# Performance work log

Hardware: AMD Instinct MI355X
Metric: run time of the kernel (lower is better)

The kernel has to match this reference:

```python
import jax, jax.numpy as jnp
import numpy as np

B, H, L, D = 8, 12, 2048, 64
E = H * D            # 768 = state_size = hidden_size
K, S, P = 3, 2, 1    # conv kernel, stride, padding (2P - K = -1 matches avg_pool residual)


def setup_inputs() -> dict:
    key = jax.random.key(0)
    ks = jax.random.split(key, 8)
    init = lambda k, shape: jax.random.normal(k, shape, jnp.float32) * 0.02
    return {
        "state": jax.random.normal(ks[0], (B, H, L, D), jnp.float32),
        # input_proj Linear(E,E)
        "Wi": init(ks[1], (E, E)), "bi": jnp.zeros((E,), jnp.float32),
        # ConvMultiheadAttention: strided Conv1d query proj, stored as [K, E_in, E_out]
        "Wq": init(ks[2], (K, E, E)), "bq": jnp.zeros((E,), jnp.float32),
        "Wk": init(ks[3], (E, E)), "bk": jnp.zeros((E,), jnp.float32),
        "Wv": init(ks[4], (E, E)), "bv": jnp.zeros((E,), jnp.float32),
        "Wao": init(ks[5], (E, E)), "bao": jnp.zeros((E,), jnp.float32),  # attn out_proj
        # output_proj Linear(E,E)
        "Wo": init(ks[6], (E, E)), "bo": jnp.zeros((E,), jnp.float32),
    }


def reference(state, Wi, bi, Wq, bq, Wk, bk, Wv, bv, Wao, bao, Wo, bo):
    b, h, l, d = state.shape
    e = h * d
    # [B,H,L,D] -> [B,L,H*D]
    x = state.transpose(0, 2, 1, 3).reshape(b, l, e)
    residual = x
    # input projection + ReLU
    x = jax.nn.relu(x @ Wi.T + bi)
    # strided convolutional query projection: [B,L,E] -> [B,Lq,E]
    q = jax.lax.conv_general_dilated(
        x, Wq, window_strides=(S,), padding=[(P, P)],
        dimension_numbers=("NWC", "WIO", "NWC")) + bq
    k = x @ Wk.T + bk
    v = x @ Wv.T + bv
    lq = q.shape[1]
    qh = q.reshape(b, lq, h, d)
    kh = k.reshape(b, l, h, d)
    vh = v.reshape(b, l, h, d)
    scale = 1.0 / jnp.sqrt(jnp.asarray(d, x.dtype))
    scores = jnp.einsum("bqhd,bkhd->bhqk", qh, kh) * scale  # [B,H,Lq,L]
    attn = jax.nn.softmax(scores, axis=-1)
    o = jnp.einsum("bhqk,bkhd->bqhd", attn, vh).reshape(b, lq, e)
    o = o @ Wao.T + bao          # attention out_proj
    o = jax.nn.relu(o)
    o = o @ Wo.T + bo            # output projection
    # avg_pool1d with kernel=1, stride=S, pad=0 == strided subsampling
    o = o + residual[:, ::S, :]
    # [B,Lq,E] -> [B,H,Lq,D]
    out = o.reshape(b, lq, h, d).transpose(0, 2, 1, 3)
    return out
```

## Files before the change

kernel.cpp:

```cpp
#include <hip/hip_runtime.h>
#include <hip/hip_bf16.h>
#include <stdint.h>

#define DEVI __device__ __forceinline__

typedef short s8v __attribute__((ext_vector_type(8)));
typedef float f4v __attribute__((ext_vector_type(4)));

DEVI short f2bf(float f) {
  unsigned u = __builtin_bit_cast(unsigned, f);
  u += 0x7FFFu + ((u >> 16) & 1u);
  return (short)(u >> 16);
}

DEVI void gload16(const void* g, void* l) {
  __builtin_amdgcn_global_load_lds((const __attribute__((address_space(1))) unsigned*)g,
                                   (__attribute__((address_space(3))) unsigned*)l,
                                   16, 0, 0);
}


__global__ __launch_bounds__(256) void k_tr_state(const float* __restrict__ st,
                                                  short* __restrict__ xbf) {
  int idx = blockIdx.x * 256 + threadIdx.x;
  int dc = idx & 7;
  int l  = (idx >> 3) & 2047;
  int hb = idx >> 14;
  int h = hb % 12, b = hb / 12;
  const float* s = st + ((size_t)hb * 2048 + l) * 64 + dc * 8;
  f4v a = *(const f4v*)s;
  f4v c = *(const f4v*)(s + 4);
  short o[8];
#pragma unroll
  for (int j = 0; j < 4; ++j) { o[j] = f2bf(a[j]); o[4 + j] = f2bf(c[j]); }
  *(s8v*)(xbf + ((size_t)(b * 2048 + l)) * 768 + h * 64 + dc * 8) = *(s8v*)o;
}

__global__ __launch_bounds__(256) void k_castw(const float* __restrict__ src,
                                               short* __restrict__ dst) {
  int idx = blockIdx.x * 256 + threadIdx.x;
  const float* s = src + (size_t)idx * 8;
  f4v a = *(const f4v*)s;
  f4v c = *(const f4v*)(s + 4);
  short o[8];
#pragma unroll
  for (int j = 0; j < 4; ++j) { o[j] = f2bf(a[j]); o[4 + j] = f2bf(c[j]); }
  *(s8v*)(dst + (size_t)idx * 8) = *(s8v*)o;
}

__global__ __launch_bounds__(256) void k_tr_wq(const float* __restrict__ wq,
                                               short* __restrict__ wqt) {
  __shared__ float tile[32][33];
  const int kw = blockIdx.z;
  const int i0 = blockIdx.y * 32, o0 = blockIdx.x * 32;
  const int tx = threadIdx.x & 31, ty = threadIdx.x >> 5;
#pragma unroll
  for (int rr = 0; rr < 32; rr += 8)
    tile[ty + rr][tx] = wq[((size_t)kw * 768 + i0 + ty + rr) * 768 + o0 + tx];
  __syncthreads();
#pragma unroll
  for (int rr = 0; rr < 32; rr += 8)
    wqt[(size_t)(o0 + ty + rr) * 2304 + kw * 768 + i0 + tx] = f2bf(tile[tx][ty + rr]);
}

__global__ __launch_bounds__(256) void k_tr_v(const short* __restrict__ v,
                                              short* __restrict__ vt) {
  __shared__ short tile[32][33];
  const int bh = blockIdx.z;
  const int l0 = blockIdx.x * 32, d0 = blockIdx.y * 32;
  const int b = bh / 12, h = bh % 12;
  const int tx = threadIdx.x & 31, ty = threadIdx.x >> 5;
#pragma unroll
  for (int rr = 0; rr < 32; rr += 8)
    tile[ty + rr][tx] = v[((size_t)(b * 2048 + l0 + ty + rr)) * 768 + h * 64 + d0 + tx];
  __syncthreads();
#pragma unroll
  for (int rr = 0; rr < 32; rr += 8)
    vt[((size_t)(bh * 64 + d0 + ty + rr)) * 2048 + l0 + tx] = tile[tx][ty + rr];
}

template <int AMODE, int EPI>
__global__ __launch_bounds__(256, 2)
void k_gemm(const short* __restrict__ A, const short* __restrict__ Bt,
            const float* __restrict__ bias, short* __restrict__ Cbf,
            float* __restrict__ Cf, const float* __restrict__ st,
            const short* __restrict__ zp, int M, int N, int K) {
  __shared__ __align__(16) short As[128 * 32];
  __shared__ __align__(16) short Bs[128 * 32];
  const int tid = threadIdx.x;
  const int w = tid >> 6, l = tid & 63;
  const int g = l >> 4, r = l & 15;

  const int nwg = gridDim.x * gridDim.y;
  const int lin = blockIdx.y * gridDim.x + blockIdx.x;
  const int lin2 = (lin & 7) * (nwg >> 3) + (lin >> 3);
  const int m0 = (lin2 / gridDim.x) * 128, n0 = (lin2 % gridDim.x) * 128;
  const int wm = w >> 1, wn = w & 1;

  f4v acc[4][4] = {};

  const int srow = 16 * w + (l >> 2);
  const int sc8 = 8 * (l & 3);

  const int nsteps = K >> 5;
  for (int ks = 0; ks < nsteps; ++ks) {
    const int kk = ks << 5;
    __syncthreads();
    if (AMODE == 0) {
      const short* a0 = A + ((size_t)(m0 + srow) * K + kk + sc8);
      gload16(a0, (char*)As + w * 1024);
      gload16(a0 + (size_t)64 * K, (char*)As + w * 1024 + 4096);
    } else {
      const int kw = ks / 24;
      const int ii = (ks - kw * 24) * 32 + sc8;
#pragma unroll
      for (int j = 0; j < 2; ++j) {
        int m = m0 + srow + 64 * j;
        int b = m >> 10, t = m & 1023;
        int lpos = 2 * t - 1 + kw;
        const short* a0 = (lpos < 0) ? (zp + sc8)
                                     : A + ((size_t)(b * 2048 + lpos) * 768 + ii);
        gload16(a0, (char*)As + w * 1024 + j * 4096);
      }
    }
    {
      const short* b0 = Bt + ((size_t)(n0 + srow) * K + kk + sc8);
      gload16(b0, (char*)Bs + w * 1024);
      gload16(b0 + (size_t)64 * K, (char*)Bs + w * 1024 + 4096);
    }
    __syncthreads();
    s8v af[4], bfr[4];
#pragma unroll
    for (int mt = 0; mt < 4; ++mt)
      af[mt] = *(const s8v*)&As[(64 * wm + 16 * mt + r) * 32 + 8 * g];
#pragma unroll
    for (int nt = 0; nt < 4; ++nt)
      bfr[nt] = *(const s8v*)&Bs[(64 * wn + 16 * nt + r) * 32 + 8 * g];
#pragma unroll
    for (int mt = 0; mt < 4; ++mt)
#pragma unroll
      for (int nt = 0; nt < 4; ++nt)
        acc[mt][nt] = __builtin_amdgcn_mfma_f32_16x16x32_bf16(af[mt], bfr[nt],
                                                              acc[mt][nt], 0, 0, 0);
  }
#pragma unroll
  for (int nt = 0; nt < 4; ++nt) {
    const int col = n0 + 64 * wn + 16 * nt + r;
    const float bv = bias[col];
#pragma unroll
    for (int mt = 0; mt < 4; ++mt) {
#pragma unroll
      for (int i = 0; i < 4; ++i) {
        int row = m0 + 64 * wm + 16 * mt + 4 * g + i;
        float v = acc[mt][nt][i] + bv;
        if (EPI == 0) v = fmaxf(v, 0.f);
        if (EPI <= 1) {
          Cbf[(size_t)row * N + col] = f2bf(v);
        } else {
          int b = row >> 10, t = row & 1023;
          int h = col >> 6, dd = col & 63;
          float res = st[(((size_t)(b * 12 + h) * 2048) + 2 * t) * 64 + dd];
          Cf[(((size_t)(b * 12 + h) * 1024) + t) * 64 + dd] = v + res;
        }
      }
    }
  }
}

__global__ __launch_bounds__(256, 3)
void k_attn(const short* __restrict__ qb, const short* __restrict__ kb,
            const short* __restrict__ vt, short* __restrict__ ob) {
  __shared__ __align__(16) short Qs[64 * 64];
  __shared__ __align__(16) short Ks[64 * 64];
  __shared__ __align__(16) short Vts[64 * 64];
  __shared__ __align__(16) short Ps[4][16 * 72];

  const int lin = blockIdx.x;
  const int blk = (lin & 7) * (1536 >> 3) + (lin >> 3);
  const int qblk = blk & 15, bh = blk >> 4;
  const int b = bh / 12, h = bh % 12;
  const int tid = threadIdx.x;
  const int w = tid >> 6, l = tid & 63;
  const int g = l >> 4, r = l & 15;

  const int row = tid >> 3, p = tid & 7;

#pragma unroll
  for (int j = 0; j < 2; ++j) {
    int rw = row + 32 * j;
    int c = p ^ (rw & 7);
    gload16(qb + ((size_t)(b * 1024 + qblk * 64 + rw) * 768 + h * 64 + 8 * c),
            (char*)Qs + w * 1024 + j * 4096);
  }
  __syncthreads();
  s8v qf[2];
#pragma unroll
  for (int c = 0; c < 2; ++c)
    qf[c] = *(const s8v*)&Qs[(16 * w + r) * 64 + 8 * ((4 * c + g) ^ (r & 7))];

  f4v oacc[4] = {};
  float mrun[4], lrun[4];
#pragma unroll
  for (int i = 0; i < 4; ++i) { mrun[i] = -1e30f; lrun[i] = 0.f; }

  for (int jb = 0; jb < 32; ++jb) {
    __syncthreads();
#pragma unroll
    for (int iss = 0; iss < 2; ++iss) {
      int jr = row + 32 * iss;
      int c = p ^ (jr & 7);
      gload16(kb + ((size_t)(b * 2048 + jb * 64 + jr) * 768 + h * 64 + 8 * c),
              (char*)Ks + w * 1024 + iss * 4096);
      gload16(vt + ((size_t)(bh * 64 + jr) * 2048 + jb * 64 + 8 * c),
              (char*)Vts + w * 1024 + iss * 4096);
    }
    __syncthreads();

    f4v sacc[4] = {};
#pragma unroll
    for (int nt = 0; nt < 4; ++nt)
#pragma unroll
      for (int c = 0; c < 2; ++c) {
        s8v kf = *(const s8v*)&Ks[(16 * nt + r) * 64 + 8 * ((4 * c + g) ^ (r & 7))];
        sacc[nt] = __builtin_amdgcn_mfma_f32_16x16x32_bf16(qf[c], kf, sacc[nt], 0, 0, 0);
      }

    float alpha[4];
#pragma unroll
    for (int i = 0; i < 4; ++i) {
      float s0 = sacc[0][i] * 0.125f, s1 = sacc[1][i] * 0.125f;
      float s2 = sacc[2][i] * 0.125f, s3 = sacc[3][i] * 0.125f;
      float mx = fmaxf(fmaxf(s0, s1), fmaxf(s2, s3));
      mx = fmaxf(mx, __shfl_xor(mx, 1));
      mx = fmaxf(mx, __shfl_xor(mx, 2));
      mx = fmaxf(mx, __shfl_xor(mx, 4));
      mx = fmaxf(mx, __shfl_xor(mx, 8));
      float mn = fmaxf(mrun[i], mx);
      alpha[i] = __expf(mrun[i] - mn);
      mrun[i] = mn;
      float p0 = __expf(s0 - mn), p1 = __expf(s1 - mn);
      float p2 = __expf(s2 - mn), p3 = __expf(s3 - mn);
      float ps = (p0 + p1) + (p2 + p3);
      ps += __shfl_xor(ps, 1);
      ps += __shfl_xor(ps, 2);
      ps += __shfl_xor(ps, 4);
      ps += __shfl_xor(ps, 8);
      lrun[i] = lrun[i] * alpha[i] + ps;
      const int qr = (4 * g + i) * 72 + r;
      Ps[w][qr] = f2bf(p0);
      Ps[w][qr + 16] = f2bf(p1);
      Ps[w][qr + 32] = f2bf(p2);
      Ps[w][qr + 48] = f2bf(p3);
    }
#pragma unroll
    for (int nt = 0; nt < 4; ++nt)
#pragma unroll
      for (int i = 0; i < 4; ++i) oacc[nt][i] *= alpha[i];

    asm volatile("" ::: "memory");
    s8v pf[2];
#pragma unroll
    for (int kc = 0; kc < 2; ++kc)
      pf[kc] = *(const s8v*)&Ps[w][r * 72 + 32 * kc + 8 * g];
#pragma unroll
    for (int nt = 0; nt < 4; ++nt)
#pragma unroll
      for (int kc = 0; kc < 2; ++kc) {
        s8v vf = *(const s8v*)&Vts[(16 * nt + r) * 64 + 8 * ((4 * kc + g) ^ (r & 7))];
        oacc[nt] = __builtin_amdgcn_mfma_f32_16x16x32_bf16(pf[kc], vf, oacc[nt], 0, 0, 0);
      }
  }

  float inv[4];
#pragma unroll
  for (int i = 0; i < 4; ++i) inv[i] = 1.f / lrun[i];
#pragma unroll
  for (int nt = 0; nt < 4; ++nt)
#pragma unroll
    for (int i = 0; i < 4; ++i) {
      int q = qblk * 64 + 16 * w + 4 * g + i;
      ob[((size_t)(b * 1024 + q)) * 768 + h * 64 + 16 * nt + r] = f2bf(oacc[nt][i] * inv[i]);
    }
}

extern "C" void kernel_launch(void* const* d_in, const int* in_sizes, int n_in,
                              void* d_out, int out_size, void* d_ws, size_t ws_size,
                              hipStream_t stream) {
  const float* state = (const float*)d_in[0];
  const float* Wi  = (const float*)d_in[1];
  const float* bi  = (const float*)d_in[2];
  const float* Wq  = (const float*)d_in[3];
  const float* bq  = (const float*)d_in[4];
  const float* Wk  = (const float*)d_in[5];
  const float* bk  = (const float*)d_in[6];
  const float* Wv  = (const float*)d_in[7];
  const float* bv  = (const float*)d_in[8];
  const float* Wao = (const float*)d_in[9];
  const float* bao = (const float*)d_in[10];
  const float* Wo  = (const float*)d_in[11];
  const float* bo  = (const float*)d_in[12];
  float* out = (float*)d_out;

  char* ws = (char*)d_ws;
  const size_t SZ = (size_t)16384 * 768 * 2;
  short* xbf = (short*)ws;
  short* y   = (short*)(ws + SZ);
  short* kbf = (short*)(ws + 2 * SZ);
  short* vbf = (short*)(ws + 3 * SZ);
  short* qbf = (short*)(ws + 4 * SZ);
  char*  wp  = ws + 4 * SZ + SZ / 2;
  short* wib  = (short*)wp;
  short* wkb  = (short*)(wp + 1 * 1179648);
  short* wvb  = (short*)(wp + 2 * 1179648);
  short* waob = (short*)(wp + 3 * 1179648);
  short* wob  = (short*)(wp + 4 * 1179648);
  short* wqt  = (short*)(wp + 5 * 1179648);
  short* zp   = (short*)(wp + 5 * 1179648 + 3538944);
  short* vtb   = xbf;
  short* attno = y;
  short* z1    = (short*)((char*)y + SZ / 2);

  hipMemsetAsync(zp, 0, 256, stream);
  k_tr_state<<<6144, 256, 0, stream>>>(state, xbf);
  k_castw<<<288, 256, 0, stream>>>(Wi, wib);
  k_castw<<<288, 256, 0, stream>>>(Wk, wkb);
  k_castw<<<288, 256, 0, stream>>>(Wv, wvb);
  k_castw<<<288, 256, 0, stream>>>(Wao, waob);
  k_castw<<<288, 256, 0, stream>>>(Wo, wob);
  k_tr_wq<<<dim3(24, 24, 3), 256, 0, stream>>>(Wq, wqt);

  k_gemm<0, 0><<<dim3(6, 128), 256, 0, stream>>>(xbf, wib, bi, y, nullptr, nullptr, zp, 16384, 768, 768);
  k_gemm<0, 1><<<dim3(6, 128), 256, 0, stream>>>(y, wkb, bk, kbf, nullptr, nullptr, zp, 16384, 768, 768);
  k_gemm<0, 1><<<dim3(6, 128), 256, 0, stream>>>(y, wvb, bv, vbf, nullptr, nullptr, zp, 16384, 768, 768);
  k_gemm<1, 1><<<dim3(6, 64), 256, 0, stream>>>(y, wqt, bq, qbf, nullptr, nullptr, zp, 8192, 768, 2304);
  k_tr_v<<<dim3(64, 2, 96), 256, 0, stream>>>(vbf, vtb);
  k_attn<<<1536, 256, 0, stream>>>(qbf, kbf, vtb, attno);
  k_gemm<0, 0><<<dim3(6, 64), 256, 0, stream>>>(attno, waob, bao, z1, nullptr, nullptr, zp, 8192, 768, 768);
  k_gemm<0, 2><<<dim3(6, 64), 256, 0, stream>>>(z1, wob, bo, nullptr, out, state, zp, 8192, 768, 768);
}
```

Baseline: 496.9 us.

## Double-buffer K/V tiles and transpose MFMA roles in attention kernel

The attention kernel now double-buffers K and V tiles in LDS, so the next tile is prefetched while the current one is computed, with one barrier per iteration instead of two. The MFMA operands are swapped so each lane owns a single query row. This turns the softmax max and sum reductions into two cross-lane shuffles, and the output can be written as packed 4-element stores. Q is loaded straight from global into registers, and rescaling of the accumulator is skipped when the running max grows by 8 or less (lazy rescale). This doubles K/V LDS use, which may affect occupancy, and relies on the deferred max staying numerically safe.

```diff
diff --git a/kernel.cpp b/kernel.cpp
--- a/kernel.cpp
+++ b/kernel.cpp
@@ -5,6 +5,7 @@
 #define DEVI __device__ __forceinline__
 
 typedef short s8v __attribute__((ext_vector_type(8)));
+typedef short s4v __attribute__((ext_vector_type(4)));
 typedef float f4v __attribute__((ext_vector_type(4)));
 
 DEVI short f2bf(float f) {
@@ -170,92 +171,92 @@
 __global__ __launch_bounds__(256, 3)
 void k_attn(const short* __restrict__ qb, const short* __restrict__ kb,
             const short* __restrict__ vt, short* __restrict__ ob) {
-  __shared__ __align__(16) short Qs[64 * 64];
-  __shared__ __align__(16) short Ks[64 * 64];
-  __shared__ __align__(16) short Vts[64 * 64];
+  __shared__ __align__(16) short Ks[2][64 * 64];
+  __shared__ __align__(16) short Vts[2][64 * 64];
   __shared__ __align__(16) short Ps[4][16 * 72];
 
   const int lin = blockIdx.x;
-  const int blk = (lin & 7) * (1536 >> 3) + (lin >> 3);
+  const int blk = (lin & 7) * 192 + (lin >> 3);
   const int qblk = blk & 15, bh = blk >> 4;
   const int b = bh / 12, h = bh % 12;
   const int tid = threadIdx.x;
   const int w = tid >> 6, l = tid & 63;
   const int g = l >> 4, r = l & 15;
-
   const int row = tid >> 3, p = tid & 7;
 
-#pragma unroll
-  for (int j = 0; j < 2; ++j) {
-    int rw = row + 32 * j;
-    int c = p ^ (rw & 7);
-    gload16(qb + ((size_t)(b * 1024 + qblk * 64 + rw) * 768 + h * 64 + 8 * c),
-            (char*)Qs + w * 1024 + j * 4096);
-  }
-  __syncthreads();
+  const short* qrow = qb + ((size_t)(b * 1024 + qblk * 64 + 16 * w + r)) * 768 + h * 64;
   s8v qf[2];
-#pragma unroll
-  for (int c = 0; c < 2; ++c)
-    qf[c] = *(const s8v*)&Qs[(16 * w + r) * 64 + 8 * ((4 * c + g) ^ (r & 7))];
-
-  f4v oacc[4] = {};
-  float mrun[4], lrun[4];
-#pragma unroll
-  for (int i = 0; i < 4; ++i) { mrun[i] = -1e30f; lrun[i] = 0.f; }
-
-  for (int jb = 0; jb < 32; ++jb) {
-    __syncthreads();
+  qf[0] = *(const s8v*)(qrow + 8 * g);
+  qf[1] = *(const s8v*)(qrow + 32 + 8 * g);
+
+  auto STAGE = [&](int buf, int jb) {
 #pragma unroll
     for (int iss = 0; iss < 2; ++iss) {
       int jr = row + 32 * iss;
       int c = p ^ (jr & 7);
-      gload16(kb + ((size_t)(b * 2048 + jb * 64 + jr) * 768 + h * 64 + 8 * c),
-              (char*)Ks + w * 1024 + iss * 4096);
-      gload16(vt + ((size_t)(bh * 64 + jr) * 2048 + jb * 64 + 8 * c),
-              (char*)Vts + w * 1024 + iss * 4096);
-    }
-    __syncthreads();
+      gload16(kb + ((size_t)(b * 2048 + jb * 64 + jr)) * 768 + h * 64 + 8 * c,
+              (char*)Ks[buf] + iss * 4096 + w * 1024);
+      gload16(vt + ((size_t)(bh * 64 + jr)) * 2048 + jb * 64 + 8 * c,
+              (char*)Vts[buf] + iss * 4096 + w * 1024);
+    }
+  };
+
+  f4v oacc[4] = {};
+  float mrun = -3.0e38f, lrun = 0.f;
+
+  STAGE(0, 0);
+  asm volatile("s_waitcnt vmcnt(0)" ::: "memory");
+  __builtin_amdgcn_s_barrier();
+
+  for (int jb = 0; jb < 32; ++jb) {
+    const int cur = jb & 1;
+    if (jb < 31) STAGE(cur ^ 1, jb + 1);
 
     f4v sacc[4] = {};
 #pragma unroll
     for (int nt = 0; nt < 4; ++nt)
 #pragma unroll
       for (int c = 0; c < 2; ++c) {
-        s8v kf = *(const s8v*)&Ks[(16 * nt + r) * 64 + 8 * ((4 * c + g) ^ (r & 7))];
-        sacc[nt] = __builtin_amdgcn_mfma_f32_16x16x32_bf16(qf[c], kf, sacc[nt], 0, 0, 0);
-      }
-
-    float alpha[4];
-#pragma unroll
-    for (int i = 0; i < 4; ++i) {
-      float s0 = sacc[0][i] * 0.125f, s1 = sacc[1][i] * 0.125f;
-      float s2 = sacc[2][i] * 0.125f, s3 = sacc[3][i] * 0.125f;
-      float mx = fmaxf(fmaxf(s0, s1), fmaxf(s2, s3));
-      mx = fmaxf(mx, __shfl_xor(mx, 1));
-      mx = fmaxf(mx, __shfl_xor(mx, 2));
-      mx = fmaxf(mx, __shfl_xor(mx, 4));
-      mx = fmaxf(mx, __shfl_xor(mx, 8));
-      float mn = fmaxf(mrun[i], mx);
-      alpha[i] = __expf(mrun[i] - mn);
-      mrun[i] = mn;
-      float p0 = __expf(s0 - mn), p1 = __expf(s1 - mn);
-      float p2 = __expf(s2 - mn), p3 = __expf(s3 - mn);
-      float ps = (p0 + p1) + (p2 + p3);
-      ps += __shfl_xor(ps, 1);
-      ps += __shfl_xor(ps, 2);
-      ps += __shfl_xor(ps, 4);
-      ps += __shfl_xor(ps, 8);
-      lrun[i] = lrun[i] * alpha[i] + ps;
-      const int qr = (4 * g + i) * 72 + r;
-      Ps[w][qr] = f2bf(p0);
-      Ps[w][qr + 16] = f2bf(p1);
-      Ps[w][qr + 32] = f2bf(p2);
-      Ps[w][qr + 48] = f2bf(p3);
-    }
+        s8v kf = *(const s8v*)&Ks[cur][(16 * nt + r) * 64 + 8 * ((4 * c + g) ^ (r & 7))];
+        sacc[nt] = __builtin_amdgcn_mfma_f32_16x16x32_bf16(kf, qf[c], sacc[nt], 0, 0, 0);
+      }
+
+    float s[16];
+    float mx = -3.0e38f;
 #pragma unroll
     for (int nt = 0; nt < 4; ++nt)
 #pragma unroll
-      for (int i = 0; i < 4; ++i) oacc[nt][i] *= alpha[i];
+      for (int i = 0; i < 4; ++i) {
+        s[4 * nt + i] = sacc[nt][i] * 0.125f;
+        mx = fmaxf(mx, s[4 * nt + i]);
+      }
+    mx = fmaxf(mx, __shfl_xor(mx, 16));
+    mx = fmaxf(mx, __shfl_xor(mx, 32));
+
+    bool defer = __all(mx <= mrun + 8.0f);
+    float mn = defer ? mrun : fmaxf(mrun, mx);
+    float alpha = defer ? 1.0f : __expf(mrun - mn);
+    mrun = mn;
+
+    float ls = 0.f;
+#pragma unroll
+    for (int k = 0; k < 8; ++k) {
+      float p0 = __expf(s[2 * k] - mn);
+      float p1 = __expf(s[2 * k + 1] - mn);
+      ls += p0 + p1;
+      unsigned pw = ((unsigned)(unsigned short)f2bf(p1) << 16) |
+                    (unsigned)(unsigned short)f2bf(p0);
+      *(unsigned*)&Ps[w][r * 72 + 16 * (k >> 1) + 4 * g + 2 * (k & 1)] = pw;
+    }
+    ls += __shfl_xor(ls, 16);
+    ls += __shfl_xor(ls, 32);
+    lrun = lrun * alpha + ls;
+    if (!defer) {
+#pragma unroll
+      for (int mt = 0; mt < 4; ++mt)
+#pragma unroll
+        for (int i = 0; i < 4; ++i) oacc[mt][i] *= alpha;
+    }
 
     asm volatile("" ::: "memory");
     s8v pf[2];
@@ -263,24 +264,26 @@
     for (int kc = 0; kc < 2; ++kc)
       pf[kc] = *(const s8v*)&Ps[w][r * 72 + 32 * kc + 8 * g];
 #pragma unroll
-    for (int nt = 0; nt < 4; ++nt)
+    for (int mt = 0; mt < 4; ++mt)
 #pragma unroll
       for (int kc = 0; kc < 2; ++kc) {
-        s8v vf = *(const s8v*)&Vts[(16 * nt + r) * 64 + 8 * ((4 * kc + g) ^ (r & 7))];
-        oacc[nt] = __builtin_amdgcn_mfma_f32_16x16x32_bf16(pf[kc], vf, oacc[nt], 0, 0, 0);
-      }
+        s8v vf = *(const s8v*)&Vts[cur][(16 * mt + r) * 64 + 8 * ((4 * kc + g) ^ (r & 7))];
+        oacc[mt] = __builtin_amdgcn_mfma_f32_16x16x32_bf16(vf, pf[kc], oacc[mt], 0, 0, 0);
+      }
+
+    asm volatile("s_waitcnt vmcnt(0)" ::: "memory");
+    __builtin_amdgcn_s_barrier();
   }
 
-  float inv[4];
-#pragma unroll
-  for (int i = 0; i < 4; ++i) inv[i] = 1.f / lrun[i];
-#pragma unroll
-  for (int nt = 0; nt < 4; ++nt)
-#pragma unroll
-    for (int i = 0; i < 4; ++i) {
-      int q = qblk * 64 + 16 * w + 4 * g + i;
-      ob[((size_t)(b * 1024 + q)) * 768 + h * 64 + 16 * nt + r] = f2bf(oacc[nt][i] * inv[i]);
-    }
+  const float inv = 1.f / lrun;
+  short* obase = ob + ((size_t)(b * 1024 + qblk * 64 + 16 * w + r)) * 768 + h * 64;
+#pragma unroll
+  for (int mt = 0; mt < 4; ++mt) {
+    short o4[4];
+#pragma unroll
+    for (int i = 0; i < 4; ++i) o4[i] = f2bf(oacc[mt][i] * inv);
+    *(s4v*)(obase + 16 * mt + 4 * g) = *(s4v*)o4;
+  }
 }
 
 extern "C" void kernel_launch(void* const* d_in, const int* in_sizes, int n_in,
```

Measured after the change: 438.9 us. 1.13x faster.
